# Kernel tuning notes

Hardware: AMD Instinct MI355X
Metric: run time of the kernel (lower is better)

## Reference

```python
import jax, jax.numpy as jnp
import numpy as np

B, N, F, D, TOPK, EXTRA = 32, 128, 10, 64, 20, 25
BN = B * N
EPS = 1e-5
SLOPE = 0.2  # GDN GraphLayer leaky_relu negative slope


def _cosine(a, b):
    na = jnp.maximum(jnp.linalg.norm(a, axis=-1), 1e-12)
    nb = jnp.maximum(jnp.linalg.norm(b, axis=-1), 1e-12)
    return (a @ b.T) / (na[:, None] * nb[None, :])


def _segment_softmax(logits, seg, num):
    m = jax.ops.segment_max(logits, seg, num_segments=num)
    m = jnp.where(jnp.isfinite(m), m, 0.0)  # empty segments
    e = jnp.exp(logits - m[seg])
    s = jax.ops.segment_sum(e, seg, num_segments=num)
    return e / jnp.maximum(s[seg], 1e-12)


def setup_inputs() -> dict:
    key = jax.random.key(0)
    ks = jax.random.split(key, 12)
    r = lambda i, shape, s=1.0: jax.random.normal(ks[i], shape, dtype=jnp.float32) * s
    return dict(
        data=r(0, (B, N, F)),
        emb=r(1, (N, D)) * 0.3,                       # nn.Embedding(node_num, dim)
        W1=r(2, (F, D)) * (1.0 / np.sqrt(F)),         # GraphLayer lin
        att_i1=r(3, (2 * D,)) * 0.1,                  # att on concat(h, emb)
        att_j1=r(4, (2 * D,)) * 0.1,
        bias1=jnp.zeros((D,), jnp.float32),
        bn1_g=jnp.ones((D,), jnp.float32),
        bn1_b=jnp.zeros((D,), jnp.float32),
        P=r(5, (BN, BN)) * (1.0 / np.sqrt(BN)),       # extra_pram
        W2=r(6, (D, D)) * (1.0 / np.sqrt(D)),         # GraphLayer1 lin
        att_i2=r(7, (D,)) * 0.1,
        att_j2=r(8, (D,)) * 0.1,
        bias2=jnp.zeros((D,), jnp.float32),
        bnO_g=jnp.ones((D,), jnp.float32),
        bnO_b=jnp.zeros((D,), jnp.float32),
        W_out=r(9, (D, 1)) * (1.0 / np.sqrt(D)),      # OutLayer Linear(dim,1)
        b_out=jnp.zeros((1,), jnp.float32),
        org_edge_index=jnp.zeros((2, 2), jnp.int32),  # dead arg in original forward
    )


def _forward(data, emb, W1, att_i1, att_j1, bias1, bn1_g, bn1_b, P, W2,
             att_i2, att_j2, bias2, bnO_g, bnO_b, W_out, b_out):
    x = data.reshape(BN, F)

    # ---- learned top-k graph from detached embedding cosine similarity ----
    w = jax.lax.stop_gradient(emb)              # weights_arr = detach()
    cos = _cosine(w, w)                         # [N, N]
    topv, topi = jax.lax.top_k(cos, TOPK)       # [N, TOPK]
    cos_w = jnp.tile(topv.reshape(-1), B)       # [B*N*TOPK]
    src0 = topi.reshape(-1)                     # gated_j (source)
    dst0 = jnp.repeat(jnp.arange(N), TOPK)      # gated_i (target)
    offs = jnp.repeat(jnp.arange(B) * N, N * TOPK)
    src = jnp.tile(src0, B) + offs
    dst = jnp.tile(dst0, B) + offs

    # ---- GraphLayer (GAT-style with embedding keys, edge weight = cos) ----
    all_emb = jnp.tile(emb, (B, 1))             # [BN, D]
    h = x @ W1                                  # [BN, D]
    kf = jnp.concatenate([h, all_emb], axis=-1) # [BN, 2D]
    si, sj = kf @ att_i1, kf @ att_j1           # [BN]
    score = jax.nn.leaky_relu(si[dst] + sj[src], SLOPE) * cos_w
    alpha = _segment_softmax(score, dst, BN)
    agg = jax.ops.segment_sum(h[src] * alpha[:, None], dst, num_segments=BN) + bias1
    mu, var = agg.mean(0), agg.var(0)           # BatchNorm1d (batch stats)
    gcn = jax.nn.relu(bn1_g * (agg - mu) / jnp.sqrt(var + EPS) + bn1_b)

    # ---- extra-feature branch (always taken: P is [BN, BN]) ----
    ef = P.T @ gcn                              # (gcn_out.T @ P).T
    g = jnp.concatenate([gcn, ef], axis=0)      # [2BN, D]
    cos2 = _cosine(g, g)                        # [2BN, 2BN]
    topv2, topi2 = jax.lax.top_k(cos2, EXTRA)
    corrs = topv2[:BN].reshape(-1)              # [BN*EXTRA]
    src2 = jnp.repeat(jnp.arange(BN), EXTRA)    # extra_i = edge_index[0] (source)
    dst2 = topi2[:BN].reshape(-1)               # extra_j = edge_index[1] (target)

    # ---- GraphLayer1 (no embedding keys, no BN in GNNLayer1.forward) ----
    h2 = g @ W2                                 # [2BN, D]
    s2 = jax.nn.leaky_relu((h2 @ att_i2)[dst2] + (h2 @ att_j2)[src2], SLOPE) * corrs
    alpha2 = _segment_softmax(s2, dst2, 2 * BN)
    agg2 = jax.ops.segment_sum(h2[src2] * alpha2[:, None], dst2, num_segments=2 * BN) + bias2
    gcn2 = jax.nn.relu(agg2)[:BN]

    # ---- output head: mul by embedding, BN over channels, Linear(D,1) ----
    x3 = gcn2.reshape(B, N, D) * emb[None]      # [B, N, D]
    mu2, var2 = x3.mean((0, 1)), x3.var((0, 1)) # BatchNorm1d over channel D
    x4 = jax.nn.relu(bnO_g * (x3 - mu2) / jnp.sqrt(var2 + EPS) + bnO_b)
    out = x4 @ W_out + b_out                    # [B, N, 1]; dropout = identity (eval)
    return out.reshape(-1, N)                   # [B, N]


def reference(data, emb, W1, att_i1, att_j1, bias1, bn1_g, bn1_b, P, W2,
              att_i2, att_j2, bias2, bnO_g, bnO_b, W_out, b_out, org_edge_index):
    # org_edge_index is dead in the original forward (only cached, never consumed)
    return _forward(data, emb, W1, att_i1, att_j1, bias1, bn1_g, bn1_b, P, W2,
                    att_i2, att_j2, bias2, bnO_g, bnO_b, W_out, b_out)
```

## Files before the change

### kernel.cpp

```cpp
#include <hip/hip_runtime.h>
#include <hip/hip_bf16.h>
#include <math.h>

#define DEV __device__ __forceinline__

constexpr int Bb   = 32;
constexpr int Nn   = 128;
constexpr int Ff   = 10;
constexpr int Dd   = 64;
constexpr int TOPK = 20;
constexpr int EXTRA= 25;
constexpr int BN   = 4096;
constexpr int TBN  = 8192;
constexpr int RC   = 16;
constexpr int CAND_CAP = 1024;
constexpr float EPS   = 1e-5f;
constexpr float SLOPE = 0.2f;

DEV unsigned int fenc(float f){
  unsigned int b = __float_as_uint(f);
  return (b & 0x80000000u) ? ~b : (b | 0x80000000u);
}
DEV float fdec(unsigned int u){
  unsigned int b = (u & 0x80000000u) ? (u & 0x7FFFFFFFu) : ~u;
  return __uint_as_float(b);
}

__global__ void k_zero(float* __restrict__ p, int n){
  int i = blockIdx.x*256 + threadIdx.x;
  if(i < n) p[i] = 0.f;
}

__global__ void k_emb_norm(const float* __restrict__ emb, float* __restrict__ norms){
  int i = blockIdx.x, d = threadIdx.x;
  float v = emb[i*Dd + d];
  float s = v*v;
  for(int o=32;o>0;o>>=1) s += __shfl_down(s, o, 64);
  if(d==0) norms[i] = fmaxf(sqrtf(s), 1e-12f);
}

__global__ void k_emb_topk(const float* __restrict__ emb, const float* __restrict__ norms,
                           float* __restrict__ topv, int* __restrict__ topi){
  __shared__ float se[Dd];
  __shared__ float sc[Nn];
  __shared__ float rv[Nn];
  __shared__ int   ri[Nn];
  int i = blockIdx.x, t = threadIdx.x;
  if(t < Dd) se[t] = emb[i*Dd + t];
  __syncthreads();
  float dot = 0.f;
  for(int d=0; d<Dd; d++) dot += se[d]*emb[t*Dd + d];
  sc[t] = dot/(norms[i]*norms[t]);
  __syncthreads();
  for(int k=0; k<TOPK; k++){
    rv[t] = sc[t]; ri[t] = t; __syncthreads();
    for(int o=Nn/2; o>0; o>>=1){
      if(t < o){
        float v2 = rv[t+o]; int i2 = ri[t+o];
        if(v2 > rv[t] || (v2 == rv[t] && i2 < ri[t])){ rv[t]=v2; ri[t]=i2; }
      }
      __syncthreads();
    }
    if(t==0){
      topv[i*TOPK + k] = rv[0];
      topi[i*TOPK + k] = ri[0];
      sc[ri[0]] = -INFINITY;
    }
    __syncthreads();
  }
}

__global__ void k_h1(const float* __restrict__ data, const float* __restrict__ emb,
                     const float* __restrict__ W1, const float* __restrict__ ai1,
                     const float* __restrict__ aj1,
                     float* __restrict__ h, float* __restrict__ si, float* __restrict__ sj){
  int r = blockIdx.x, d = threadIdx.x;
  int node = r & (Nn-1);
  __shared__ float xr[Ff];
  if(d < Ff) xr[d] = data[r*Ff + d];
  __syncthreads();
  float hv = 0.f;
  #pragma unroll
  for(int f=0; f<Ff; f++) hv += xr[f]*W1[f*Dd + d];
  h[r*Dd + d] = hv;
  float e = emb[node*Dd + d];
  float a = hv*ai1[d] + e*ai1[Dd + d];
  float b = hv*aj1[d] + e*aj1[Dd + d];
  for(int o=32;o>0;o>>=1){ a += __shfl_down(a,o,64); b += __shfl_down(b,o,64); }
  if(d==0){ si[r] = a; sj[r] = b; }
}

__global__ void k_agg1(const float* __restrict__ h, const float* __restrict__ si,
                       const float* __restrict__ sj, const float* __restrict__ topv,
                       const int* __restrict__ topi, const float* __restrict__ bias1,
                       float* __restrict__ agg){
  int r = blockIdx.x, d = threadIdx.x;
  int b = r >> 7, node = r & (Nn-1);
  __shared__ float sal[TOPK];
  __shared__ int   ssrc[TOPK];
  if(d < TOPK){
    int s = b*Nn + topi[node*TOPK + d];
    float sc = si[r] + sj[s];
    sc = sc >= 0.f ? sc : SLOPE*sc;
    sal[d] = sc * topv[node*TOPK + d];
    ssrc[d] = s;
  }
  __syncthreads();
  float m = -INFINITY;
  #pragma unroll
  for(int k=0;k<TOPK;k++) m = fmaxf(m, sal[k]);
  float al[TOPK]; float ssum = 0.f;
  #pragma unroll
  for(int k=0;k<TOPK;k++){ al[k] = expf(sal[k]-m); ssum += al[k]; }
  float inv = 1.0f/fmaxf(ssum, 1e-12f);
  float acc = 0.f;
  #pragma unroll
  for(int k=0;k<TOPK;k++) acc += al[k]*inv*h[ssrc[k]*Dd + d];
  agg[r*Dd + d] = acc + bias1[d];
}

__global__ void k_colstats(const float* __restrict__ x, float* __restrict__ mu, float* __restrict__ var){
  int c = blockIdx.x, t = threadIdx.x;
  float s = 0.f, s2 = 0.f;
  for(int r=t; r<BN; r+=256){ float v = x[r*Dd + c]; s += v; s2 += v*v; }
  __shared__ float ls[256], ls2[256];
  ls[t]=s; ls2[t]=s2; __syncthreads();
  for(int o=128;o>0;o>>=1){
    if(t<o){ ls[t]+=ls[t+o]; ls2[t]+=ls2[t+o]; }
    __syncthreads();
  }
  if(t==0){ float m = ls[0]/BN; mu[c]=m; var[c]=ls2[0]/BN - m*m; }
}

__global__ void k_bnrelu1(const float* __restrict__ agg, const float* __restrict__ mu,
                          const float* __restrict__ var, const float* __restrict__ gamma,
                          const float* __restrict__ beta, float* __restrict__ g){
  int idx = blockIdx.x*256 + threadIdx.x;
  int c = idx & (Dd-1);
  float v = agg[idx];
  float y = gamma[c]*(v - mu[c])/sqrtf(var[c]+EPS) + beta[c];
  g[idx] = fmaxf(y, 0.f);
}

__global__ __launch_bounds__(256) void k_ef1(const float* __restrict__ P, const float* __restrict__ gcn,
                                             float* __restrict__ part){
  __shared__ float Pt[16*64];
  __shared__ float Gt[16*64];
  int t = threadIdx.x;
  int jbase = blockIdx.x*64;
  int r0 = blockIdx.y*256;
  int row = t >> 4, col4 = (t & 15)*4;
  int tr = t >> 4, tc = t & 15;
  float acc[4][4] = {};
  for(int step=0; step<16; step++){
    int r = r0 + step*16;
    float4 pv = *(const float4*)&P[(size_t)(r+row)*BN + jbase + col4];
    float4 gv = *(const float4*)&gcn[(r+row)*Dd + col4];
    __syncthreads();
    *(float4*)&Pt[row*64 + col4] = pv;
    *(float4*)&Gt[row*64 + col4] = gv;
    __syncthreads();
    #pragma unroll
    for(int rr=0; rr<16; rr++){
      float4 pa = *(float4*)&Pt[rr*64 + tr*4];
      float4 gb = *(float4*)&Gt[rr*64 + tc*4];
      float pav[4] = {pa.x, pa.y, pa.z, pa.w};
      float gbv[4] = {gb.x, gb.y, gb.z, gb.w};
      #pragma unroll
      for(int a=0;a<4;a++)
        #pragma unroll
        for(int b=0;b<4;b++) acc[a][b] += pav[a]*gbv[b];
    }
  }
  float* dst = part + ((size_t)blockIdx.y*BN + jbase)*Dd;
  #pragma unroll
  for(int a=0;a<4;a++){
    float4 v = make_float4(acc[a][0],acc[a][1],acc[a][2],acc[a][3]);
    *(float4*)&dst[(tr*4+a)*Dd + tc*4] = v;
  }
}

__global__ void k_ef2(const float* __restrict__ part, float* __restrict__ ef){
  int i = blockIdx.x*256 + threadIdx.x;
  float4 s = make_float4(0.f,0.f,0.f,0.f);
  #pragma unroll
  for(int c=0;c<RC;c++){
    float4 v = *(const float4*)&part[(size_t)c*BN*Dd + (size_t)i*4];
    s.x += v.x; s.y += v.y; s.z += v.z; s.w += v.w;
  }
  *(float4*)&ef[(size_t)i*4] = s;
}

__global__ void k_rownorm(const float* __restrict__ x, float* __restrict__ nrm){
  int r = blockIdx.x, d = threadIdx.x;
  float v = x[(size_t)r*Dd + d];
  float s = v*v;
  for(int o=32;o>0;o>>=1) s += __shfl_down(s, o, 64);
  if(d==0) nrm[r] = fmaxf(sqrtf(s), 1e-12f);
}

__global__ __launch_bounds__(256) void k_sgemm(const float* __restrict__ g, const float* __restrict__ gnorm,
                                               int rbase, float* __restrict__ S){
  __shared__ float A[64*128];
  __shared__ float Bs[64*128];
  int t = threadIdx.x;
  int ctile = blockIdx.x*128;
  int rtile = rbase + blockIdx.y*128;
  int q = t >> 4, m0 = t & 15;
  #pragma unroll
  for(int l=0;l<8;l++){
    int m = m0 + 16*l;
    float ia = 1.0f/gnorm[rtile + m];
    float ib = 1.0f/gnorm[ctile + m];
    float4 av = *(const float4*)&g[(size_t)(rtile+m)*Dd + q*4];
    float4 bv = *(const float4*)&g[(size_t)(ctile+m)*Dd + q*4];
    A[(q*4+0)*128 + m] = av.x*ia; A[(q*4+1)*128 + m] = av.y*ia;
    A[(q*4+2)*128 + m] = av.z*ia; A[(q*4+3)*128 + m] = av.w*ia;
    Bs[(q*4+0)*128 + m] = bv.x*ib; Bs[(q*4+1)*128 + m] = bv.y*ib;
    Bs[(q*4+2)*128 + m] = bv.z*ib; Bs[(q*4+3)*128 + m] = bv.w*ib;
  }
  __syncthreads();
  int tr = t >> 4;
  int tc = t & 15;
  float acc[8][8] = {};
  #pragma unroll 4
  for(int k=0;k<64;k++){
    float a[8], b[8];
    #pragma unroll
    for(int i=0;i<8;i++) a[i] = A[k*128 + tr + 16*i];
    #pragma unroll
    for(int j=0;j<8;j++) b[j] = Bs[k*128 + tc + 16*j];
    #pragma unroll
    for(int i=0;i<8;i++)
      #pragma unroll
      for(int j=0;j<8;j++) acc[i][j] += a[i]*b[j];
  }
  int rloc = blockIdx.y*128;
  #pragma unroll
  for(int i=0;i<8;i++){
    int r = rloc + tr + 16*i;
    #pragma unroll
    for(int j=0;j<8;j++)
      S[(size_t)r*TBN + ctile + tc + 16*j] = acc[i][j];
  }
}

__global__ __launch_bounds__(256) void k_radix(const float* __restrict__ S, int rbase,
                                               float* __restrict__ topv2, int* __restrict__ topi2){
  __shared__ unsigned hist[4096];
  __shared__ unsigned wtot[4];
  __shared__ unsigned candE[CAND_CAP];
  __shared__ unsigned short candC[CAND_CAP];
  __shared__ unsigned bc_bin, bc_need, bc_cnt, bc_c;
  int t = threadIdx.x;
  int lane = t & 63, wid = t >> 6;
  int r = blockIdx.x;
  const float* src = S + (size_t)r*TBN;
  int col0 = t*32;
  unsigned enc[32];
  #pragma unroll
  for(int j=0;j<8;j++){
    float4 v = *(const float4*)&src[col0 + j*4];
    enc[j*4+0]=fenc(v.x); enc[j*4+1]=fenc(v.y); enc[j*4+2]=fenc(v.z); enc[j*4+3]=fenc(v.w);
  }
  #pragma unroll
  for(int j=0;j<16;j++) hist[t*16 + j] = 0u;
  __syncthreads();
  #pragma unroll
  for(int j=0;j<32;j++) atomicAdd(&hist[enc[j] >> 20], 1u);
  __syncthreads();
  unsigned lsum = 0u;
  #pragma unroll
  for(int j=0;j<16;j++) lsum += hist[t*16 + j];
  unsigned v = lsum;
  #pragma unroll
  for(int o=1;o<64;o<<=1){
    unsigned u = (unsigned)__shfl_down((int)v, o, 64);
    if(lane + o < 64) v += u;
  }
  if(lane == 0) wtot[wid] = v;
  __syncthreads();
  unsigned cross = 0u;
  #pragma unroll
  for(int w2=0;w2<4;w2++) if(w2 > wid) cross += wtot[w2];
  unsigned Tinc = v + cross;
  unsigned above = Tinc - lsum;
  unsigned run = above;
  #pragma unroll
  for(int b=15;b>=0;b--){
    unsigned prev = run;
    run += hist[t*16 + b];
    if(run >= EXTRA && prev < EXTRA){ bc_bin = (unsigned)(t*16 + b); bc_need = EXTRA - prev; }
  }
  if(t==0){ bc_cnt = 0u; bc_c = 0u; }
  __syncthreads();
  unsigned pivotBin = bc_bin, needIn = bc_need;
  int gr = rbase + r;
  #pragma unroll
  for(int j=0;j<32;j++){
    unsigned e = enc[j];
    unsigned bin = e >> 20;
    if(bin > pivotBin){
      unsigned s = atomicAdd(&bc_cnt, 1u);
      topv2[gr*EXTRA + s] = fdec(e);
      topi2[gr*EXTRA + s] = col0 + j;
    } else if(bin == pivotBin){
      unsigned ci = atomicAdd(&bc_c, 1u);
      if(ci < CAND_CAP){ candE[ci] = e; candC[ci] = (unsigned short)(col0 + j); }
    }
  }
  __syncthreads();
  unsigned c = bc_c;
  if(c <= CAND_CAP){
    for(unsigned i=t; i<c; i+=256){
      unsigned ei = candE[i]; unsigned coli = candC[i];
      unsigned rank = 0;
      for(unsigned j2=0;j2<c;j2++){
        unsigned ej = candE[j2];
        rank += (ej > ei) || (ej == ei && candC[j2] < coli);
      }
      if(rank < needIn){
        unsigned s = atomicAdd(&bc_cnt, 1u);
        topv2[gr*EXTRA + s] = fdec(ei);
        topi2[gr*EXTRA + s] = (int)coli;
      }
    }
  } else {
    unsigned* h256  = hist;
    unsigned* scanb = hist + 1024;
    unsigned prefix = pivotBin;
    unsigned need = needIn;
    const int shifts[3] = {12, 4, 0};
    const unsigned masks[3] = {255u, 255u, 15u};
    const int nbins[3] = {256, 256, 16};
    for(int p=0;p<3;p++){
      int sh = shifts[p]; unsigned mk = masks[p]; int nb = nbins[p];
      if(t < nb) h256[t] = 0u;
      __syncthreads();
      #pragma unroll
      for(int j=0;j<32;j++){
        unsigned e = enc[j];
        int pshift = (p==0)? 20 : (p==1? 12 : 4);
        if((e >> pshift) == prefix) atomicAdd(&h256[(e>>sh)&mk], 1u);
      }
      __syncthreads();
      unsigned vv = (t < nb) ? h256[t] : 0u;
      for(int o=1;o<nb;o<<=1){
        if(t < nb) scanb[t] = vv;
        __syncthreads();
        if(t < nb && t+o < nb) vv += scanb[t+o];
        __syncthreads();
      }
      if(t < nb) scanb[t] = vv;
      __syncthreads();
      if(t < nb){
        unsigned nxt = (t < nb-1) ? scanb[t+1] : 0u;
        if(vv >= need && nxt < need){ bc_bin = (prefix << ((p==2)?4:8)) | (unsigned)t; bc_need = need - nxt; }
      }
      __syncthreads();
      prefix = bc_bin; need = bc_need;
      __syncthreads();
    }
    unsigned pivotEnc = prefix;
    unsigned needTies = need;
    unsigned tie_local = 0u;
    #pragma unroll
    for(int j=0;j<32;j++){
      unsigned e = enc[j];
      if((e >> 20) == pivotBin){
        if(e > pivotEnc){
          unsigned s = atomicAdd(&bc_cnt, 1u);
          topv2[gr*EXTRA + s] = fdec(e);
          topi2[gr*EXTRA + s] = col0 + j;
        } else if(e == pivotEnc) tie_local++;
      }
    }
    unsigned iv = tie_local;
    for(int o=1;o<256;o<<=1){
      scanb[t] = iv; __syncthreads();
      if(t >= o) iv += scanb[t-o];
      __syncthreads();
    }
    unsigned rank = iv - tie_local;
    #pragma unroll
    for(int j=0;j<32;j++){
      unsigned e = enc[j];
      if(e == pivotEnc && (e >> 20) == pivotBin){
        if(rank < needTies){
          unsigned s = atomicAdd(&bc_cnt, 1u);
          topv2[gr*EXTRA + s] = fdec(e);
          topi2[gr*EXTRA + s] = col0 + j;
        }
        rank++;
      }
    }
  }
}

__global__ void k_h2(const float* __restrict__ g, const float* __restrict__ W2,
                     const float* __restrict__ ai2w, const float* __restrict__ aj2w,
                     float* __restrict__ h2, float* __restrict__ a2i, float* __restrict__ a2j){
  int r = blockIdx.x, d = threadIdx.x;
  __shared__ float gr[Dd];
  gr[d] = g[(size_t)r*Dd + d];
  __syncthreads();
  float hv = 0.f;
  #pragma unroll
  for(int k=0;k<Dd;k++) hv += gr[k]*W2[k*Dd + d];
  h2[(size_t)r*Dd + d] = hv;
  float a = hv*ai2w[d];
  float b = hv*aj2w[d];
  for(int o=32;o>0;o>>=1){ a += __shfl_down(a,o,64); b += __shfl_down(b,o,64); }
  if(d==0){ a2i[r]=a; a2j[r]=b; }
}

__global__ void k_s2(const float* __restrict__ a2i, const float* __restrict__ a2j,
                     const float* __restrict__ topv2, const int* __restrict__ topi2,
                     float* __restrict__ s2, unsigned int* __restrict__ segmax){
  int e = blockIdx.x*256 + threadIdx.x;
  if(e >= BN*EXTRA) return;
  int r = e/EXTRA;
  int dst = topi2[e];
  float sc = a2i[dst] + a2j[r];
  sc = sc >= 0.f ? sc : SLOPE*sc;
  sc *= topv2[e];
  s2[e] = sc;
  atomicMax(&segmax[dst], fenc(sc));
}

__global__ void k_e2(const float* __restrict__ s2, const int* __restrict__ topi2,
                     const unsigned int* __restrict__ segmax,
                     float* __restrict__ e2, float* __restrict__ ssum){
  int e = blockIdx.x*256 + threadIdx.x;
  if(e >= BN*EXTRA) return;
  int dst = topi2[e];
  float m = fdec(segmax[dst]);
  float v = expf(s2[e] - m);
  e2[e] = v;
  atomicAdd(&ssum[dst], v);
}

__global__ void k_scat(const float* __restrict__ e2, const float* __restrict__ ssum,
                       const int* __restrict__ topi2, const float* __restrict__ h2,
                       float* __restrict__ agg2){
  int idx = blockIdx.x*256 + threadIdx.x;
  int e = idx >> 6, d = idx & 63;
  int dst = topi2[e];
  int src = e/EXTRA;
  float alpha = e2[e]/fmaxf(ssum[dst], 1e-12f);
  atomicAdd(&agg2[(size_t)dst*Dd + d], alpha*h2[(size_t)src*Dd + d]);
}

__global__ void k_headstats(const float* __restrict__ agg2, const float* __restrict__ bias2,
                            const float* __restrict__ emb, float* __restrict__ mu2, float* __restrict__ var2){
  int c = blockIdx.x, t = threadIdx.x;
  float bc = bias2[c];
  float s = 0.f, s2 = 0.f;
  for(int r=t; r<BN; r+=256){
    float v = fmaxf(agg2[(size_t)r*Dd + c] + bc, 0.f) * emb[(r & (Nn-1))*Dd + c];
    s += v; s2 += v*v;
  }
  __shared__ float ls[256], ls2[256];
  ls[t]=s; ls2[t]=s2; __syncthreads();
  for(int o=128;o>0;o>>=1){
    if(t<o){ ls[t]+=ls[t+o]; ls2[t]+=ls2[t+o]; }
    __syncthreads();
  }
  if(t==0){ float m=ls[0]/BN; mu2[c]=m; var2[c]=ls2[0]/BN - m*m; }
}

__global__ void k_out(const float* __restrict__ agg2, const float* __restrict__ bias2,
                      const float* __restrict__ emb, const float* __restrict__ mu2,
                      const float* __restrict__ var2, const float* __restrict__ gO,
                      const float* __restrict__ bO, const float* __restrict__ Wout,
                      const float* __restrict__ bout, float* __restrict__ out){
  int r = blockIdx.x, d = threadIdx.x;
  float v = fmaxf(agg2[(size_t)r*Dd + d] + bias2[d], 0.f) * emb[(r & (Nn-1))*Dd + d];
  float y = gO[d]*(v - mu2[d])/sqrtf(var2[d]+EPS) + bO[d];
  y = fmaxf(y, 0.f)*Wout[d];
  for(int o=32;o>0;o>>=1) y += __shfl_down(y, o, 64);
  if(d==0) out[r] = y + bout[0];
}

extern "C" void kernel_launch(void* const* d_in, const int* in_sizes, int n_in,
                              void* d_out, int out_size, void* d_ws, size_t ws_size,
                              hipStream_t stream){
  const float* data  = (const float*)d_in[0];
  const float* emb   = (const float*)d_in[1];
  const float* W1    = (const float*)d_in[2];
  const float* ai1   = (const float*)d_in[3];
  const float* aj1   = (const float*)d_in[4];
  const float* bias1 = (const float*)d_in[5];
  const float* bn1g  = (const float*)d_in[6];
  const float* bn1b  = (const float*)d_in[7];
  const float* P     = (const float*)d_in[8];
  const float* W2    = (const float*)d_in[9];
  const float* ai2w  = (const float*)d_in[10];
  const float* aj2w  = (const float*)d_in[11];
  const float* bias2 = (const float*)d_in[12];
  const float* bnOg  = (const float*)d_in[13];
  const float* bnOb  = (const float*)d_in[14];
  const float* Wout  = (const float*)d_in[15];
  const float* bout  = (const float*)d_in[16];
  float* out = (float*)d_out;

  char* w = (char*)d_ws;
  auto alloc = [&](size_t nbytes)->char*{
    char* p = w; w += (nbytes + 255) & ~(size_t)255; return p;
  };
  float* norms1 = (float*)alloc(Nn*4);
  float* topv1  = (float*)alloc(Nn*TOPK*4);
  int*   topi1  = (int*)  alloc(Nn*TOPK*4);
  float* h      = (float*)alloc((size_t)BN*Dd*4);
  float* si     = (float*)alloc(BN*4);
  float* sj     = (float*)alloc(BN*4);
  float* agg1   = (float*)alloc((size_t)BN*Dd*4);
  float* mu1    = (float*)alloc(Dd*4);
  float* var1   = (float*)alloc(Dd*4);
  float* g      = (float*)alloc((size_t)TBN*Dd*4);
  float* gnorm  = (float*)alloc(TBN*4);
  float* topv2  = (float*)alloc((size_t)BN*EXTRA*4);
  int*   topi2  = (int*)  alloc((size_t)BN*EXTRA*4);
  float* h2     = (float*)alloc((size_t)TBN*Dd*4);
  float* a2i    = (float*)alloc(TBN*4);
  float* a2j    = (float*)alloc(TBN*4);
  float* s2     = (float*)alloc((size_t)BN*EXTRA*4);
  float* e2     = (float*)alloc((size_t)BN*EXTRA*4);
  float* zblock = (float*)alloc(((size_t)TBN*Dd + TBN + TBN)*4);
  float* agg2   = zblock;
  float* ssum   = zblock + (size_t)TBN*Dd;
  unsigned int* segmax = (unsigned int*)(ssum + TBN);
  float* mu2    = (float*)alloc(Dd*4);
  float* var2   = (float*)alloc(Dd*4);
  float* efpart = (float*)alloc((size_t)RC*BN*Dd*4);

  size_t used = (size_t)(w - (char*)d_ws);
  size_t rem  = ws_size > used ? ws_size - used : 0;
  int chunkRows = 4096;
  while(chunkRows > 128 && (size_t)chunkRows*TBN*4 > rem) chunkRows >>= 1;
  float* Schunk = (float*)alloc((size_t)chunkRows*TBN*4);

  k_emb_norm<<<Nn, 64, 0, stream>>>(emb, norms1);
  k_emb_topk<<<Nn, Nn, 0, stream>>>(emb, norms1, topv1, topi1);
  k_h1<<<BN, 64, 0, stream>>>(data, emb, W1, ai1, aj1, h, si, sj);
  k_agg1<<<BN, 64, 0, stream>>>(h, si, sj, topv1, topi1, bias1, agg1);
  k_colstats<<<Dd, 256, 0, stream>>>(agg1, mu1, var1);
  k_bnrelu1<<<(BN*Dd)/256, 256, 0, stream>>>(agg1, mu1, var1, bn1g, bn1b, g);

  k_ef1<<<dim3(64, RC), 256, 0, stream>>>(P, g, efpart);
  k_ef2<<<(BN*Dd/4)/256, 256, 0, stream>>>(efpart, g + (size_t)BN*Dd);

  k_rownorm<<<TBN, 64, 0, stream>>>(g, gnorm);
  for(int rbase=0; rbase<BN; rbase+=chunkRows){
    k_sgemm<<<dim3(TBN/128, chunkRows/128), 256, 0, stream>>>(g, gnorm, rbase, Schunk);
    k_radix<<<chunkRows, 256, 0, stream>>>(Schunk, rbase, topv2, topi2);
  }

  k_h2<<<TBN, 64, 0, stream>>>(g, W2, ai2w, aj2w, h2, a2i, a2j);
  k_zero<<<((TBN*Dd + 2*TBN) + 255)/256, 256, 0, stream>>>(zblock, TBN*Dd + 2*TBN);
  k_s2<<<(BN*EXTRA + 255)/256, 256, 0, stream>>>(a2i, a2j, topv2, topi2, s2, segmax);
  k_e2<<<(BN*EXTRA + 255)/256, 256, 0, stream>>>(s2, topi2, segmax, e2, ssum);
  k_scat<<<(BN*EXTRA*Dd)/256, 256, 0, stream>>>(e2, ssum, topi2, h2, agg2);

  k_headstats<<<Dd, 256, 0, stream>>>(agg2, bias2, emb, mu2, var2);
  k_out<<<BN, 64, 0, stream>>>(agg2, bias2, emb, mu2, var2, bnOg, bnOb, Wout, bout, out);
}
```

Baseline: 381.4 us.

## Store similarity matrix as 16-bit keys, then refine top-k with exact recompute

```diff
diff --git a/kernel.cpp b/kernel.cpp
--- a/kernel.cpp
+++ b/kernel.cpp
@@ -12,8 +12,9 @@
 constexpr int EXTRA= 25;
 constexpr int BN   = 4096;
 constexpr int TBN  = 8192;
-constexpr int RC   = 16;
-constexpr int CAND_CAP = 1024;
+constexpr int RC   = 32;
+constexpr int CAP16 = 2048;
+constexpr int TCAP  = 256;
 constexpr float EPS   = 1e-5f;
 constexpr float SLOPE = 0.2f;
 
@@ -148,11 +149,11 @@
   __shared__ float Gt[16*64];
   int t = threadIdx.x;
   int jbase = blockIdx.x*64;
-  int r0 = blockIdx.y*256;
+  int r0 = blockIdx.y*128;
   int row = t >> 4, col4 = (t & 15)*4;
   int tr = t >> 4, tc = t & 15;
   float acc[4][4] = {};
-  for(int step=0; step<16; step++){
+  for(int step=0; step<8; step++){
     int r = r0 + step*16;
     float4 pv = *(const float4*)&P[(size_t)(r+row)*BN + jbase + col4];
     float4 gv = *(const float4*)&gcn[(r+row)*Dd + col4];
@@ -199,8 +200,8 @@
   if(d==0) nrm[r] = fmaxf(sqrtf(s), 1e-12f);
 }
 
-__global__ __launch_bounds__(256) void k_sgemm(const float* __restrict__ g, const float* __restrict__ gnorm,
-                                               int rbase, float* __restrict__ S){
+__global__ __launch_bounds__(256) void k_sgemm16(const float* __restrict__ g, const float* __restrict__ gnorm,
+                                                 int rbase, unsigned short* __restrict__ S16){
   __shared__ float A[64*128];
   __shared__ float Bs[64*128];
   int t = threadIdx.x;
@@ -241,33 +242,35 @@
     int r = rloc + tr + 16*i;
     #pragma unroll
     for(int j=0;j<8;j++)
-      S[(size_t)r*TBN + ctile + tc + 16*j] = acc[i][j];
-  }
-}
-
-__global__ __launch_bounds__(256) void k_radix(const float* __restrict__ S, int rbase,
-                                               float* __restrict__ topv2, int* __restrict__ topi2){
+      S16[(size_t)r*TBN + ctile + tc + 16*j] = (unsigned short)(fenc(acc[i][j]) >> 16);
+  }
+}
+
+__global__ __launch_bounds__(256) void k_radix16(const unsigned short* __restrict__ S16, int rbase,
+                                                 int4* __restrict__ hdr, int* __restrict__ selcols,
+                                                 int* __restrict__ tiecols){
   __shared__ unsigned hist[4096];
   __shared__ unsigned wtot[4];
-  __shared__ unsigned candE[CAND_CAP];
-  __shared__ unsigned short candC[CAND_CAP];
-  __shared__ unsigned bc_bin, bc_need, bc_cnt, bc_c;
+  __shared__ unsigned cand[CAP16];
+  __shared__ unsigned bc_bin, bc_need, bc_sure, bc_c, bc_tie, bc_n3;
   int t = threadIdx.x;
   int lane = t & 63, wid = t >> 6;
   int r = blockIdx.x;
-  const float* src = S + (size_t)r*TBN;
-  int col0 = t*32;
-  unsigned enc[32];
-  #pragma unroll
-  for(int j=0;j<8;j++){
-    float4 v = *(const float4*)&src[col0 + j*4];
-    enc[j*4+0]=fenc(v.x); enc[j*4+1]=fenc(v.y); enc[j*4+2]=fenc(v.z); enc[j*4+3]=fenc(v.w);
+  const uint4* src = (const uint4*)(S16 + (size_t)r*TBN);
+  unsigned code[32];
+  #pragma unroll
+  for(int j=0;j<4;j++){
+    uint4 u = src[t*4 + j];
+    code[j*8+0]=u.x&0xFFFFu; code[j*8+1]=u.x>>16;
+    code[j*8+2]=u.y&0xFFFFu; code[j*8+3]=u.y>>16;
+    code[j*8+4]=u.z&0xFFFFu; code[j*8+5]=u.z>>16;
+    code[j*8+6]=u.w&0xFFFFu; code[j*8+7]=u.w>>16;
   }
   #pragma unroll
   for(int j=0;j<16;j++) hist[t*16 + j] = 0u;
   __syncthreads();
   #pragma unroll
-  for(int j=0;j<32;j++) atomicAdd(&hist[enc[j] >> 20], 1u);
+  for(int j=0;j<32;j++) atomicAdd(&hist[code[j] >> 4], 1u);
   __syncthreads();
   unsigned lsum = 0u;
   #pragma unroll
@@ -292,106 +295,117 @@
     run += hist[t*16 + b];
     if(run >= EXTRA && prev < EXTRA){ bc_bin = (unsigned)(t*16 + b); bc_need = EXTRA - prev; }
   }
-  if(t==0){ bc_cnt = 0u; bc_c = 0u; }
+  if(t==0){ bc_sure = 0u; bc_c = 0u; bc_tie = 0u; bc_n3 = 0u; }
   __syncthreads();
   unsigned pivotBin = bc_bin, needIn = bc_need;
   int gr = rbase + r;
+  int col0 = t*32;
   #pragma unroll
   for(int j=0;j<32;j++){
-    unsigned e = enc[j];
-    unsigned bin = e >> 20;
+    unsigned cd = code[j];
+    unsigned bin = cd >> 4;
     if(bin > pivotBin){
-      unsigned s = atomicAdd(&bc_cnt, 1u);
-      topv2[gr*EXTRA + s] = fdec(e);
-      topi2[gr*EXTRA + s] = col0 + j;
+      unsigned s = atomicAdd(&bc_sure, 1u);
+      selcols[gr*32 + s] = col0 + j;
     } else if(bin == pivotBin){
       unsigned ci = atomicAdd(&bc_c, 1u);
-      if(ci < CAND_CAP){ candE[ci] = e; candC[ci] = (unsigned short)(col0 + j); }
+      if(ci < CAP16) cand[ci] = (cd << 13) | (unsigned)(col0 + j);
     }
   }
   __syncthreads();
   unsigned c = bc_c;
-  if(c <= CAND_CAP){
+  int flag = (c > CAP16) ? 1 : 0;
+  if(!flag){
     for(unsigned i=t; i<c; i+=256){
-      unsigned ei = candE[i]; unsigned coli = candC[i];
-      unsigned rank = 0;
+      unsigned pk = cand[i];
+      unsigned myc = pk >> 13;
+      unsigned gt = 0, eq = 0;
       for(unsigned j2=0;j2<c;j2++){
-        unsigned ej = candE[j2];
-        rank += (ej > ei) || (ej == ei && candC[j2] < coli);
-      }
-      if(rank < needIn){
-        unsigned s = atomicAdd(&bc_cnt, 1u);
-        topv2[gr*EXTRA + s] = fdec(ei);
-        topi2[gr*EXTRA + s] = (int)coli;
+        unsigned oc = cand[j2] >> 13;
+        gt += (oc > myc); eq += (oc == myc);
+      }
+      if(gt + eq <= needIn){
+        unsigned s = atomicAdd(&bc_sure, 1u);
+        selcols[gr*32 + s] = (int)(pk & 8191u);
+      } else if(gt < needIn){
+        unsigned u = atomicAdd(&bc_tie, 1u);
+        if(u < TCAP) tiecols[gr*TCAP + u] = (int)(pk & 8191u);
+        bc_n3 = needIn - gt;
+      }
+    }
+  }
+  __syncthreads();
+  if(bc_tie > TCAP) flag = 1;
+  if(t==0) hdr[gr] = make_int4((int)bc_sure, (int)(bc_tie > TCAP ? TCAP : bc_tie), (int)bc_n3, flag);
+}
+
+__global__ __launch_bounds__(64) void k_gather(const float* __restrict__ g, const float* __restrict__ gnorm,
+                                               const int4* __restrict__ hdr, const int* __restrict__ selcols,
+                                               const int* __restrict__ tiecols,
+                                               float* __restrict__ topv2, int* __restrict__ topi2){
+  __shared__ float ar[64];
+  __shared__ float rowv[TBN];
+  __shared__ unsigned tE[TCAP];
+  __shared__ int scnt;
+  int r = blockIdx.x, t = threadIdx.x;
+  int4 H = hdr[r];
+  float invr = 1.0f/gnorm[r];
+  ar[t] = g[(size_t)r*Dd + t]*invr;
+  if(t==0) scnt = 0;
+  __syncthreads();
+  auto dotc = [&](int c)->float{
+    float invc = 1.0f/gnorm[c];
+    float acc = 0.f;
+    const float* gc = g + (size_t)c*Dd;
+    for(int k=0;k<Dd;k++) acc = fmaf(ar[k], gc[k]*invc, acc);
+    return acc;
+  };
+  if(!H.w){
+    int sc = H.x, tcnt = H.y, need3 = H.z;
+    for(int i=t; i<sc; i+=64){
+      int c = selcols[r*32 + i];
+      topv2[r*EXTRA + i] = dotc(c);
+      topi2[r*EXTRA + i] = c;
+    }
+    for(int i=t; i<tcnt; i+=64) tE[i] = fenc(dotc(tiecols[r*TCAP + i]));
+    __syncthreads();
+    for(int i=t; i<tcnt; i+=64){
+      unsigned e = tE[i]; int c = tiecols[r*TCAP + i];
+      int rank = 0;
+      for(int j=0;j<tcnt;j++){
+        unsigned e2 = tE[j]; int c2 = tiecols[r*TCAP + j];
+        rank += (e2 > e) || (e2 == e && c2 < c);
+      }
+      if(rank < need3){
+        int s = sc + atomicAdd(&scnt, 1);
+        topv2[r*EXTRA + s] = fdec(e);
+        topi2[r*EXTRA + s] = c;
       }
     }
   } else {
-    unsigned* h256  = hist;
-    unsigned* scanb = hist + 1024;
-    unsigned prefix = pivotBin;
-    unsigned need = needIn;
-    const int shifts[3] = {12, 4, 0};
-    const unsigned masks[3] = {255u, 255u, 15u};
-    const int nbins[3] = {256, 256, 16};
-    for(int p=0;p<3;p++){
-      int sh = shifts[p]; unsigned mk = masks[p]; int nb = nbins[p];
-      if(t < nb) h256[t] = 0u;
-      __syncthreads();
+    for(int c=t; c<TBN; c+=64) rowv[c] = dotc(c);
+    __syncthreads();
+    float bv = -INFINITY; int bc = 0x7FFFFFFF;
+    for(int j=0;j<128;j++){
+      int c = j*64 + t; float vv = rowv[c];
+      if(vv > bv || (vv == bv && c < bc)){ bv = vv; bc = c; }
+    }
+    for(int k=0;k<EXTRA;k++){
+      float gv = bv; int gi = bc;
       #pragma unroll
-      for(int j=0;j<32;j++){
-        unsigned e = enc[j];
-        int pshift = (p==0)? 20 : (p==1? 12 : 4);
-        if((e >> pshift) == prefix) atomicAdd(&h256[(e>>sh)&mk], 1u);
-      }
-      __syncthreads();
-      unsigned vv = (t < nb) ? h256[t] : 0u;
-      for(int o=1;o<nb;o<<=1){
-        if(t < nb) scanb[t] = vv;
-        __syncthreads();
-        if(t < nb && t+o < nb) vv += scanb[t+o];
-        __syncthreads();
-      }
-      if(t < nb) scanb[t] = vv;
-      __syncthreads();
-      if(t < nb){
-        unsigned nxt = (t < nb-1) ? scanb[t+1] : 0u;
-        if(vv >= need && nxt < need){ bc_bin = (prefix << ((p==2)?4:8)) | (unsigned)t; bc_need = need - nxt; }
-      }
-      __syncthreads();
-      prefix = bc_bin; need = bc_need;
-      __syncthreads();
-    }
-    unsigned pivotEnc = prefix;
-    unsigned needTies = need;
-    unsigned tie_local = 0u;
-    #pragma unroll
-    for(int j=0;j<32;j++){
-      unsigned e = enc[j];
-      if((e >> 20) == pivotBin){
-        if(e > pivotEnc){
-          unsigned s = atomicAdd(&bc_cnt, 1u);
-          topv2[gr*EXTRA + s] = fdec(e);
-          topi2[gr*EXTRA + s] = col0 + j;
-        } else if(e == pivotEnc) tie_local++;
-      }
-    }
-    unsigned iv = tie_local;
-    for(int o=1;o<256;o<<=1){
-      scanb[t] = iv; __syncthreads();
-      if(t >= o) iv += scanb[t-o];
-      __syncthreads();
-    }
-    unsigned rank = iv - tie_local;
-    #pragma unroll
-    for(int j=0;j<32;j++){
-      unsigned e = enc[j];
-      if(e == pivotEnc && (e >> 20) == pivotBin){
-        if(rank < needTies){
-          unsigned s = atomicAdd(&bc_cnt, 1u);
-          topv2[gr*EXTRA + s] = fdec(e);
-          topi2[gr*EXTRA + s] = col0 + j;
+      for(int o=1;o<64;o<<=1){
+        float v2 = __shfl_xor(gv, o, 64); int i2 = __shfl_xor(gi, o, 64);
+        if(v2 > gv || (v2 == gv && i2 < gi)){ gv = v2; gi = i2; }
+      }
+      if(t==0){ topv2[r*EXTRA + k] = gv; topi2[r*EXTRA + k] = gi; }
+      int owner = gi & 63;
+      if(t == owner){
+        rowv[gi] = -INFINITY;
+        bv = -INFINITY; bc = 0x7FFFFFFF;
+        for(int j=0;j<128;j++){
+          int c = j*64 + t; float vv = rowv[c];
+          if(vv > bv || (vv == bv && c < bc)){ bv = vv; bc = c; }
         }
-        rank++;
       }
     }
   }
@@ -419,8 +433,9 @@
                      float* __restrict__ s2, unsigned int* __restrict__ segmax){
   int e = blockIdx.x*256 + threadIdx.x;
   if(e >= BN*EXTRA) return;
+  int dst = topi2[e];
+  if(dst >= BN) return;
   int r = e/EXTRA;
-  int dst = topi2[e];
   float sc = a2i[dst] + a2j[r];
   sc = sc >= 0.f ? sc : SLOPE*sc;
   sc *= topv2[e];
@@ -434,6 +449,7 @@
   int e = blockIdx.x*256 + threadIdx.x;
   if(e >= BN*EXTRA) return;
   int dst = topi2[e];
+  if(dst >= BN) return;
   float m = fdec(segmax[dst]);
   float v = expf(s2[e] - m);
   e2[e] = v;
@@ -446,6 +462,7 @@
   int idx = blockIdx.x*256 + threadIdx.x;
   int e = idx >> 6, d = idx & 63;
   int dst = topi2[e];
+  if(dst >= BN) return;
   int src = e/EXTRA;
   float alpha = e2[e]/fmaxf(ssum[dst], 1e-12f);
   atomicAdd(&agg2[(size_t)dst*Dd + d], alpha*h2[(size_t)src*Dd + d]);
@@ -521,15 +538,18 @@
   float* gnorm  = (float*)alloc(TBN*4);
   float* topv2  = (float*)alloc((size_t)BN*EXTRA*4);
   int*   topi2  = (int*)  alloc((size_t)BN*EXTRA*4);
-  float* h2     = (float*)alloc((size_t)TBN*Dd*4);
-  float* a2i    = (float*)alloc(TBN*4);
-  float* a2j    = (float*)alloc(TBN*4);
+  int4*  hdr    = (int4*) alloc((size_t)BN*16);
+  int*   selcols= (int*)  alloc((size_t)BN*32*4);
+  int*   tiecols= (int*)  alloc((size_t)BN*TCAP*4);
+  float* h2     = (float*)alloc((size_t)BN*Dd*4);
+  float* a2i    = (float*)alloc(BN*4);
+  float* a2j    = (float*)alloc(BN*4);
   float* s2     = (float*)alloc((size_t)BN*EXTRA*4);
   float* e2     = (float*)alloc((size_t)BN*EXTRA*4);
-  float* zblock = (float*)alloc(((size_t)TBN*Dd + TBN + TBN)*4);
+  float* zblock = (float*)alloc(((size_t)BN*Dd + BN + BN)*4);
   float* agg2   = zblock;
-  float* ssum   = zblock + (size_t)TBN*Dd;
-  unsigned int* segmax = (unsigned int*)(ssum + TBN);
+  float* ssum   = zblock + (size_t)BN*Dd;
+  unsigned int* segmax = (unsigned int*)(ssum + BN);
   float* mu2    = (float*)alloc(Dd*4);
   float* var2   = (float*)alloc(Dd*4);
   float* efpart = (float*)alloc((size_t)RC*BN*Dd*4);
@@ -537,8 +557,8 @@
   size_t used = (size_t)(w - (char*)d_ws);
   size_t rem  = ws_size > used ? ws_size - used : 0;
   int chunkRows = 4096;
-  while(chunkRows > 128 && (size_t)chunkRows*TBN*4 > rem) chunkRows >>= 1;
-  float* Schunk = (float*)alloc((size_t)chunkRows*TBN*4);
+  while(chunkRows > 128 && (size_t)chunkRows*TBN*2 > rem) chunkRows >>= 1;
+  unsigned short* S16 = (unsigned short*)alloc((size_t)chunkRows*TBN*2);
 
   k_emb_norm<<<Nn, 64, 0, stream>>>(emb, norms1);
   k_emb_topk<<<Nn, Nn, 0, stream>>>(emb, norms1, topv1, topi1);
@@ -552,12 +572,13 @@
 
   k_rownorm<<<TBN, 64, 0, stream>>>(g, gnorm);
   for(int rbase=0; rbase<BN; rbase+=chunkRows){
-    k_sgemm<<<dim3(TBN/128, chunkRows/128), 256, 0, stream>>>(g, gnorm, rbase, Schunk);
-    k_radix<<<chunkRows, 256, 0, stream>>>(Schunk, rbase, topv2, topi2);
-  }
-
-  k_h2<<<TBN, 64, 0, stream>>>(g, W2, ai2w, aj2w, h2, a2i, a2j);
-  k_zero<<<((TBN*Dd + 2*TBN) + 255)/256, 256, 0, stream>>>(zblock, TBN*Dd + 2*TBN);
+    k_sgemm16<<<dim3(TBN/128, chunkRows/128), 256, 0, stream>>>(g, gnorm, rbase, S16);
+    k_radix16<<<chunkRows, 256, 0, stream>>>(S16, rbase, hdr, selcols, tiecols);
+  }
+  k_gather<<<BN, 64, 0, stream>>>(g, gnorm, hdr, selcols, tiecols, topv2, topi2);
+
+  k_h2<<<BN, 64, 0, stream>>>(g, W2, ai2w, aj2w, h2, a2i, a2j);
+  k_zero<<<((BN*Dd + 2*BN) + 255)/256, 256, 0, stream>>>(zblock, BN*Dd + 2*BN);
   k_s2<<<(BN*EXTRA + 255)/256, 256, 0, stream>>>(a2i, a2j, topv2, topi2, s2, segmax);
   k_e2<<<(BN*EXTRA + 255)/256, 256, 0, stream>>>(s2, topi2, segmax, e2, ssum);
   k_scat<<<(BN*EXTRA*Dd)/256, 256, 0, stream>>>(e2, ssum, topi2, h2, agg2);
```

New measurement: 408.1 us. 1.07x slower.
